# Optimization experiments

Measured on AMD Instinct MI355X. Metric: run time of the kernel, lower is better.

Reference implementation:

```python
import jax, jax.numpy as jnp
import numpy as np

# Module / shape constants (match init_kwargs and forward-path constants)
H = 8          # heads
DH = 80        # dim_head
QDIM = 640     # query_dim == inner_dim (context = x, self-attention content branch)
B = 1
NQ = 2048      # query tokens
NS = 2048      # injected style tokens
T = 1.2        # injection_config['T']  (attn_matrix_scale)
GAMMA = 0.3    # injection_config['gamma'] (q_mix)
LAMBDA_MAX = 2.5
TOPK = 128     # style_topk
STYLE_SCALE = 1.0
SCALE = DH ** -0.5


def _split_heads(t, h):
    # 'b n (h d) -> (b h) n d'
    b, n, hd = t.shape
    return t.reshape(b, n, h, hd // h).transpose(0, 2, 1, 3).reshape(b * h, n, hd // h)


def setup_inputs() -> dict:
    key = jax.random.key(0)
    ks = jax.random.split(key, 9)
    x = jax.random.normal(ks[0], (B, NQ, QDIM), jnp.float32)
    Q_c_injected = jax.random.normal(ks[1], (H, NQ, DH), jnp.float32) * 0.5
    K_s_injected = jax.random.normal(ks[2], (H, NS, DH), jnp.float32) * 0.5
    V_s_injected = jax.random.normal(ks[3], (H, NS, DH), jnp.float32) * 0.5
    # Learned params (nn.Linear weights are [out, in]; no bias on q/k/v)
    Wq = jax.random.normal(ks[4], (H * DH, QDIM), jnp.float32) * 0.02
    Wk = jax.random.normal(ks[5], (H * DH, QDIM), jnp.float32) * 0.02
    Wv = jax.random.normal(ks[6], (H * DH, QDIM), jnp.float32) * 0.02
    Wo = jax.random.normal(ks[7], (QDIM, H * DH), jnp.float32) * 0.02
    bo = jnp.zeros((QDIM,), jnp.float32)
    ada_gate = jnp.array([0.2], jnp.float32)
    return {"x": x, "Q_c_injected": Q_c_injected, "K_s_injected": K_s_injected,
            "V_s_injected": V_s_injected, "Wq": Wq, "Wk": Wk, "Wv": Wv,
            "Wo": Wo, "bo": bo, "ada_gate": ada_gate}


def reference(x, Q_c_injected, K_s_injected, V_s_injected, Wq, Wk, Wv, Wo, bo, ada_gate):
    b, n, _ = x.shape
    # Projections, context = x
    q_cs = _split_heads(x @ Wq.T, H)                    # (b h) n d
    k_cs = _split_heads(x @ Wk.T, H)                    # (b h) m d
    v_cs = _split_heads(x @ Wv.T, H)
    Q_c = jnp.tile(Q_c_injected, (b, 1, 1))             # torch.cat([Q_c]*b)
    q = Q_c * GAMMA + q_cs * (1.0 - GAMMA)              # Q_hat_cs
    K_s = jnp.tile(K_s_injected, (b, 1, 1))
    V_s = jnp.tile(V_s_injected, (b, 1, 1))

    style = jnp.einsum('bid,bjd->bij', q, K_s) * (T * SCALE)   # (bh) nq ns
    content = jnp.einsum('bid,bjd->bij', q, k_cs) * SCALE       # (bh) nq nc
    ns = style.shape[-1]
    s4 = style.reshape(b, H, n, ns)
    c4 = content.reshape(b, H, n, -1)

    # Per-head logsumexp gating between style and content branches
    r = jax.scipy.special.logsumexp(s4, axis=-1) - jax.scipy.special.logsumexp(c4, axis=-1)
    r = jnp.clip(r, -20.0, 20.0).mean(axis=1)           # (b, nq)
    lam = 1.0 + (LAMBDA_MAX - 1.0) * jax.nn.sigmoid(r)  # lambda_map
    style = (s4 * lam[:, None, :, None]).reshape(b * H, n, ns)

    # Top-k sparsification of style logits (scatter top-k values onto -inf canvas)
    vals, idx = jax.lax.top_k(style, TOPK)
    neg = jnp.finfo(style.dtype).min
    bi = jnp.arange(b * H)[:, None, None]
    ni = jnp.arange(n)[None, :, None]
    style = jnp.full_like(style, neg).at[bi, ni, idx].set(vals)

    logits = jnp.concatenate([style, content], axis=-1)
    attn = jax.nn.softmax(logits, axis=-1)
    v = jnp.concatenate([V_s * STYLE_SCALE, v_cs], axis=1)      # (bh) (ns+nc) d
    out = jnp.einsum('bij,bjd->bid', attn, v)

    # AdaIN-style modulation
    A = attn.reshape(b, H, n, -1)
    Vh = v.reshape(b, H, -1, DH)
    Qh = q.reshape(b, H, n, DH)
    Vmean = jnp.einsum('bhnm,bhmd->bhnd', A, Vh)
    mu = Qh.mean(axis=2, keepdims=True)
    var = Qh.var(axis=2, keepdims=True)                 # unbiased=False
    Qn = (Qh - mu) / jnp.sqrt(var + 1e-5)
    Vsq = jnp.einsum('bhnm,bhmd->bhnd', A, Vh * Vh)
    Vstd = jnp.sqrt(jnp.clip(Vsq - Vmean ** 2, 1e-5))
    out_mod = (Vstd * Qn + Vmean).reshape(b * H, n, DH)  # use_std_scale path

    g = jnp.tanh(ada_gate[0])                            # use_residual_gate
    out = out + g * (out_mod - out)
    out = out.reshape(b, H, n, DH).transpose(0, 2, 1, 3).reshape(b, n, H * DH)
    return out @ Wo.T + bo                               # to_out (dropout=0)
```

## Files before the change

### kernel.cpp

```cpp
#include <hip/hip_runtime.h>
#include <hip/hip_fp16.h>
#include <math.h>

#define NH 8
#define DH 80
#define NTOK 2048
#define QD 640
#define SCALE_F 0.11180339887498949f
#define TSCALE_F (1.2f * SCALE_F)
#define GAMMA_F 0.3f
#define LMAX_F 2.5f
#define TOPKN 128

typedef __attribute__((ext_vector_type(8))) short bf16x8;
typedef __attribute__((ext_vector_type(4))) float f32x4;
typedef __attribute__((ext_vector_type(4))) unsigned short u16x4;

#define OFF_QB   0u
#define OFF_OB   1310720u
#define OFF_QH   2621440u
#define OFF_QL   3407872u
#define OFF_KCH  4194304u
#define OFF_KSH  4980736u
#define OFF_KSL  5767168u
#define OFF_VCT  6553600u
#define OFF_VCQT 7208960u
#define OFF_VST  7864320u
#define OFF_VSQT 8519680u
#define OFF_OP   9175040u
#define OFF_SP   14417920u
#define OFF_DEN  19660800u
#define OFF_MSZ  19726336u
#define OFF_LSZ  19791872u
#define OFF_MCZ  19857408u
#define OFF_LCZ  19922944u
#define OFF_M    19988480u
#define OFF_LAM  20004864u
#define OFF_THR  20006912u
#define OFF_MU   20023296u
#define OFF_RSTD 20023936u
#define OFF_S16  20024576u
#define OFF_SC16 36801792u

static __device__ __forceinline__ unsigned short f2bf(float f) {
  unsigned u = __float_as_uint(f);
  return (unsigned short)((u + 0x7FFFu + ((u >> 16) & 1u)) >> 16);
}
static __device__ __forceinline__ float bf2f(unsigned short s) {
  return __uint_as_float(((unsigned)s) << 16);
}
static __device__ __forceinline__ unsigned sk16(unsigned u) {
  return (u & 0x8000u) ? (~u & 0xFFFFu) : (u | 0x8000u);
}

__global__ __launch_bounds__(256) void k_projmm(
    const float* __restrict__ x, const float* __restrict__ Wq,
    const float* __restrict__ Wk, const float* __restrict__ Wv,
    const float* __restrict__ Qc, float* __restrict__ qb,
    unsigned short* __restrict__ qh_, unsigned short* __restrict__ ql_,
    unsigned short* __restrict__ kch_,
    unsigned short* __restrict__ vct_, unsigned short* __restrict__ vcqt_)
{
  const float* W = (blockIdx.z == 0) ? Wq : ((blockIdx.z == 1) ? Wk : Wv);
  const int n0 = blockIdx.y * 64, c0 = blockIdx.x * 64;
  const int tid = threadIdx.x;
  const int w = tid >> 6, l = tid & 63;
  const int cc = l & 15, g = l >> 4;
  const bool full3 = (blockIdx.z == 0);

  __shared__ unsigned short sXh[64 * 72];
  __shared__ unsigned short sXl[64 * 72];
  __shared__ unsigned short sWh[64 * 72];
  __shared__ unsigned short sWl[64 * 72];

  f32x4 D[4];
#pragma unroll
  for (int ct = 0; ct < 4; ++ct) D[ct] = (f32x4){0.f, 0.f, 0.f, 0.f};

  for (int k0 = 0; k0 < QD; k0 += 64) {
    __syncthreads();
#pragma unroll
    for (int it = 0; it < 4; ++it) {
      int f = tid + it * 256;
      int row = f >> 4, col4 = f & 15;
      float4 xa = *(const float4*)(x + (size_t)(n0 + row) * QD + k0 + col4 * 4);
      float4 wa = *(const float4*)(W + (size_t)(c0 + row) * QD + k0 + col4 * 4);
      u16x4 xh, xl, wh, wl;
      float xv[4] = {xa.x, xa.y, xa.z, xa.w};
      float wv[4] = {wa.x, wa.y, wa.z, wa.w};
#pragma unroll
      for (int j = 0; j < 4; ++j) {
        unsigned short h1 = f2bf(xv[j]);
        xh[j] = h1; xl[j] = f2bf(xv[j] - bf2f(h1));
        unsigned short h2 = f2bf(wv[j]);
        wh[j] = h2; wl[j] = f2bf(wv[j] - bf2f(h2));
      }
      *(u16x4*)&sXh[row * 72 + col4 * 4] = xh;
      *(u16x4*)&sXl[row * 72 + col4 * 4] = xl;
      *(u16x4*)&sWh[row * 72 + col4 * 4] = wh;
      *(u16x4*)&sWl[row * 72 + col4 * 4] = wl;
    }
    __syncthreads();
    bf16x8 ah[2], al[2];
#pragma unroll
    for (int kc = 0; kc < 2; ++kc) {
      ah[kc] = *(const bf16x8*)&sXh[(w * 16 + cc) * 72 + kc * 32 + g * 8];
      al[kc] = *(const bf16x8*)&sXl[(w * 16 + cc) * 72 + kc * 32 + g * 8];
    }
#pragma unroll
    for (int ct = 0; ct < 4; ++ct) {
#pragma unroll
      for (int kc = 0; kc < 2; ++kc) {
        bf16x8 bh = *(const bf16x8*)&sWh[(ct * 16 + cc) * 72 + kc * 32 + g * 8];
        bf16x8 bl = *(const bf16x8*)&sWl[(ct * 16 + cc) * 72 + kc * 32 + g * 8];
        D[ct] = __builtin_amdgcn_mfma_f32_16x16x32_bf16(ah[kc], bh, D[ct], 0, 0, 0);
        D[ct] = __builtin_amdgcn_mfma_f32_16x16x32_bf16(ah[kc], bl, D[ct], 0, 0, 0);
        if (full3)
          D[ct] = __builtin_amdgcn_mfma_f32_16x16x32_bf16(al[kc], bh, D[ct], 0, 0, 0);
      }
    }
  }
#pragma unroll
  for (int ct = 0; ct < 4; ++ct) {
#pragma unroll
    for (int r = 0; r < 4; ++r) {
      int n = n0 + w * 16 + g * 4 + r;
      int ccol = c0 + ct * 16 + cc;
      int h = ccol / DH, d = ccol - h * DH;
      size_t i80 = ((size_t)h * NTOK + n) * 80 + d;
      size_t i96 = ((size_t)h * NTOK + n) * 96 + d;
      float val = D[ct][r];
      if (blockIdx.z == 0) {
        val = GAMMA_F * Qc[i80] + (1.f - GAMMA_F) * val;
        qb[i80] = val;
        unsigned short hs = f2bf(val);
        qh_[i96] = hs;
        ql_[i96] = f2bf(val - bf2f(hs));
      } else if (blockIdx.z == 1) {
        kch_[i96] = f2bf(val);
      } else {
        size_t iT = (((size_t)h * 80 + d) << 11) + n;
        vct_[iT]  = f2bf(val);
        vcqt_[iT] = f2bf(val * val);
      }
    }
  }
}

__global__ __launch_bounds__(256) void k_cvt(
    const float* __restrict__ Ks, const float* __restrict__ Vs,
    unsigned short* __restrict__ Ksh, unsigned short* __restrict__ Ksl,
    unsigned short* __restrict__ VTs, unsigned short* __restrict__ VTqs,
    unsigned short* __restrict__ qh_, unsigned short* __restrict__ ql_,
    unsigned short* __restrict__ kch_)
{
  const int h = blockIdx.y;
  const int n0 = blockIdx.x * 64;
  const int tid = threadIdx.x;
  __shared__ unsigned short sVT[80 * 68];
  __shared__ unsigned short sVQ[80 * 68];

  for (int f = tid; f < 1280; f += 256) {
    int rr = f / 20, dc = f % 20;
    size_t i80 = ((size_t)h * NTOK + n0 + rr) * 80 + dc * 4;
    size_t i96 = ((size_t)h * NTOK + n0 + rr) * 96 + dc * 4;
    float4 kv = *(const float4*)(Ks + i80);
    float kvv[4] = {kv.x, kv.y, kv.z, kv.w};
    u16x4 kh, kl;
#pragma unroll
    for (int j = 0; j < 4; ++j) {
      unsigned short hs = f2bf(kvv[j]);
      kh[j] = hs; kl[j] = f2bf(kvv[j] - bf2f(hs));
    }
    *(u16x4*)(Ksh + i96) = kh;
    *(u16x4*)(Ksl + i96) = kl;
    float4 vv = *(const float4*)(Vs + i80);
    float vvv[4] = {vv.x, vv.y, vv.z, vv.w};
#pragma unroll
    for (int j = 0; j < 4; ++j) {
      int d = dc * 4 + j;
      sVT[d * 68 + rr] = f2bf(vvv[j]);
      sVQ[d * 68 + rr] = f2bf(vvv[j] * vvv[j]);
    }
  }
  for (int f = tid; f < 1024; f += 256) {
    int rr = f >> 4, dcol = 80 + (f & 15);
    size_t i96 = ((size_t)h * NTOK + n0 + rr) * 96 + dcol;
    Ksh[i96] = 0; Ksl[i96] = 0; qh_[i96] = 0; ql_[i96] = 0; kch_[i96] = 0;
  }
  __syncthreads();
  for (int f = tid; f < 640; f += 256) {
    int d = f >> 3, kp8 = f & 7;
    size_t iT = (((size_t)h * 80 + d) << 11) + n0 + kp8 * 8;
    *(bf16x8*)(VTs + iT)  = *(const bf16x8*)&sVT[d * 68 + kp8 * 8];
    *(bf16x8*)(VTqs + iT) = *(const bf16x8*)&sVQ[d * 68 + kp8 * 8];
  }
}

__global__ __launch_bounds__(128) void k_qstats(
    const float* __restrict__ qb, float* __restrict__ mu, float* __restrict__ rstd)
{
  const int h = blockIdx.x / DH, d = blockIdx.x % DH;
  const int tid = threadIdx.x;
  float s = 0.f, s2 = 0.f;
  for (int n = tid; n < NTOK; n += 128) {
    float v = qb[((size_t)h * NTOK + n) * 80 + d];
    s += v; s2 = fmaf(v, v, s2);
  }
#pragma unroll
  for (int off = 32; off; off >>= 1) { s += __shfl_xor(s, off, 64); s2 += __shfl_xor(s2, off, 64); }
  __shared__ float sh[4];
  if ((tid & 63) == 0) { sh[(tid >> 6) * 2] = s; sh[(tid >> 6) * 2 + 1] = s2; }
  __syncthreads();
  if (tid == 0) {
    float S = sh[0] + sh[2], S2 = sh[1] + sh[3];
    float mval = S * (1.f / NTOK);
    float var = S2 * (1.f / NTOK) - mval * mval;
    mu[h * DH + d] = mval;
    rstd[h * DH + d] = rsqrtf(var + 1e-5f);
  }
}

__global__ __launch_bounds__(256) void k_passA(
    const unsigned short* __restrict__ qh_, const unsigned short* __restrict__ ql_,
    const unsigned short* __restrict__ Ksh, const unsigned short* __restrict__ Ksl,
    const unsigned short* __restrict__ kch_,
    unsigned short* __restrict__ S16, unsigned short* __restrict__ Sc16,
    float* __restrict__ mSz, float* __restrict__ lSz,
    float* __restrict__ mCz, float* __restrict__ lCz)
{
  const int bid = blockIdx.x;
  const int swz = (bid & 7) * 128 + (bid >> 3);
  const int q0 = (swz & 31) * 64;
  const int h  = (swz >> 5) & 7;
  const int z  = swz >> 8;
  const int tid = threadIdx.x;
  const int w = tid >> 6, l = tid & 63;
  const int c = l & 15, g = l >> 4;

  __shared__ unsigned short sKh[64 * 104];
  __shared__ unsigned short sKl[64 * 104];
  __shared__ unsigned short sS[4 * 16 * 68];
  unsigned short* sSw = sS + w * 16 * 68;
  const int orow = l >> 2, oq = l & 3;

  bf16x8 qhf[3], qlf[3];
  {
    const size_t qrow = ((size_t)h * NTOK + q0 + w * 16 + c) * 96;
#pragma unroll
    for (int kc = 0; kc < 3; ++kc) {
      qhf[kc] = *(const bf16x8*)(qh_ + qrow + kc * 32 + g * 8);
      qlf[kc] = *(const bf16x8*)(ql_ + qrow + kc * 32 + g * 8);
    }
  }
  float m[4], lse[4], mc[4], lc[4];
#pragma unroll
  for (int r = 0; r < 4; ++r) { m[r] = -INFINITY; lse[r] = 0.f; mc[r] = -INFINITY; lc[r] = 0.f; }

  for (int t = 0; t < 8; ++t) {
    const size_t kbase = ((size_t)h * NTOK + z * 512 + t * 64) * 96;
    __syncthreads();
    for (int f = tid; f < 768; f += 256) {
      int row = f / 12, ch = f % 12;
      *(bf16x8*)(sKh + row * 104 + ch * 8) = *(const bf16x8*)(Ksh + kbase + row * 96 + ch * 8);
      *(bf16x8*)(sKl + row * 104 + ch * 8) = *(const bf16x8*)(Ksl + kbase + row * 96 + ch * 8);
    }
    __syncthreads();
#pragma unroll
    for (int ct = 0; ct < 4; ++ct) {
      f32x4 D = {0.f, 0.f, 0.f, 0.f};
      const int krow = (ct * 16 + c) * 104 + g * 8;
#pragma unroll
      for (int kc = 0; kc < 3; ++kc) {
        bf16x8 bh = *(const bf16x8*)(sKh + krow + kc * 32);
        D = __builtin_amdgcn_mfma_f32_16x16x32_bf16(qhf[kc], bh, D, 0, 0, 0);
      }
#pragma unroll
      for (int kc = 0; kc < 3; ++kc) {
        bf16x8 bl = *(const bf16x8*)(sKl + krow + kc * 32);
        D = __builtin_amdgcn_mfma_f32_16x16x32_bf16(qhf[kc], bl, D, 0, 0, 0);
      }
#pragma unroll
      for (int kc = 0; kc < 3; ++kc) {
        bf16x8 bh = *(const bf16x8*)(sKh + krow + kc * 32);
        D = __builtin_amdgcn_mfma_f32_16x16x32_bf16(qlf[kc], bh, D, 0, 0, 0);
      }
#pragma unroll
      for (int r = 0; r < 4; ++r) {
        float s = D[r] * TSCALE_F;
        sSw[(g * 4 + r) * 68 + ct * 16 + c] = __half_as_ushort(__float2half(s));
        lse[r] += __expf(s);
        m[r] = fmaxf(m[r], s);
      }
    }
    {
      size_t gbase = ((size_t)h * NTOK + q0 + w * 16 + orow) * 2048 + z * 512 + t * 64 + oq * 16;
      *(uint4*)(S16 + gbase)     = *(const uint4*)&sSw[orow * 68 + oq * 16];
      *(uint4*)(S16 + gbase + 8) = *(const uint4*)&sSw[orow * 68 + oq * 16 + 8];
    }
  }
  for (int t = 0; t < 8; ++t) {
    const size_t kbase = ((size_t)h * NTOK + z * 512 + t * 64) * 96;
    __syncthreads();
    for (int f = tid; f < 768; f += 256) {
      int row = f / 12, ch = f % 12;
      *(bf16x8*)(sKh + row * 104 + ch * 8) = *(const bf16x8*)(kch_ + kbase + row * 96 + ch * 8);
    }
    __syncthreads();
#pragma unroll
    for (int ct = 0; ct < 4; ++ct) {
      f32x4 D = {0.f, 0.f, 0.f, 0.f};
      const int krow = (ct * 16 + c) * 104 + g * 8;
#pragma unroll
      for (int kc = 0; kc < 3; ++kc) {
        bf16x8 bh = *(const bf16x8*)(sKh + krow + kc * 32);
        D = __builtin_amdgcn_mfma_f32_16x16x32_bf16(qhf[kc], bh, D, 0, 0, 0);
      }
#pragma unroll
      for (int r = 0; r < 4; ++r) {
        float s = D[r] * SCALE_F;
        sSw[(g * 4 + r) * 68 + ct * 16 + c] = __half_as_ushort(__float2half(s));
        lc[r] += __expf(s);
        mc[r] = fmaxf(mc[r], s);
      }
    }
    {
      size_t gbase = ((size_t)h * NTOK + q0 + w * 16 + orow) * 2048 + z * 512 + t * 64 + oq * 16;
      *(uint4*)(Sc16 + gbase)     = *(const uint4*)&sSw[orow * 68 + oq * 16];
      *(uint4*)(Sc16 + gbase + 8) = *(const uint4*)&sSw[orow * 68 + oq * 16 + 8];
    }
  }
#pragma unroll
  for (int off = 1; off < 16; off <<= 1) {
#pragma unroll
    for (int r = 0; r < 4; ++r) {
      lse[r] += __shfl_xor(lse[r], off, 64);
      m[r] = fmaxf(m[r], __shfl_xor(m[r], off, 64));
      lc[r] += __shfl_xor(lc[r], off, 64);
      mc[r] = fmaxf(mc[r], __shfl_xor(mc[r], off, 64));
    }
  }
  if (c == 0) {
    size_t base = (size_t)(z * 8 + h) * NTOK + q0 + w * 16 + g * 4;
#pragma unroll
    for (int r = 0; r < 4; ++r) {
      mSz[base + r] = m[r]; lSz[base + r] = lse[r];
      mCz[base + r] = mc[r]; lCz[base + r] = lc[r];
    }
  }
}

__global__ __launch_bounds__(256) void k_gate(
    const float* __restrict__ mSz, const float* __restrict__ lSz,
    const float* __restrict__ mCz, const float* __restrict__ lCz,
    float* __restrict__ M_, float* __restrict__ lam_)
{
  int n = blockIdx.x * 256 + threadIdx.x;
  if (n >= NTOK) return;
  float msf[NH], mcf[NH], sum = 0.f;
#pragma unroll
  for (int h = 0; h < NH; ++h) {
    float mm = -INFINITY, cm = -INFINITY, ls = 0.f, lcs = 0.f;
#pragma unroll
    for (int zz = 0; zz < 4; ++zz) {
      mm = fmaxf(mm, mSz[(size_t)(zz * 8 + h) * NTOK + n]);
      cm = fmaxf(cm, mCz[(size_t)(zz * 8 + h) * NTOK + n]);
      ls  += lSz[(size_t)(zz * 8 + h) * NTOK + n];
      lcs += lCz[(size_t)(zz * 8 + h) * NTOK + n];
    }
    float lse_s = __logf(ls);
    float lse_c = __logf(lcs);
    msf[h] = mm; mcf[h] = cm;
    sum += fminf(fmaxf(lse_s - lse_c, -20.f), 20.f);
  }
  float lam = 1.f + (LMAX_F - 1.f) * (1.f / (1.f + __expf(-sum * (1.f / NH))));
  lam_[n] = lam;
#pragma unroll
  for (int h = 0; h < NH; ++h)
    M_[h * NTOK + n] = fmaxf(lam * msf[h], mcf[h]);
}

__global__ __launch_bounds__(512) void k_topk(const unsigned short* __restrict__ S16,
                                              unsigned* __restrict__ thr_)
{
  const int h = blockIdx.y;
  const int n = blockIdx.x * 8 + (threadIdx.x >> 6);
  const int l = threadIdx.x & 63;
  const unsigned short* Srow = S16 + ((size_t)h * NTOK + n) * 2048;
  unsigned kv[32];
#pragma unroll
  for (int t = 0; t < 4; ++t) {
    uint4 v = ((const uint4*)Srow)[t * 64 + l];
    unsigned dw[4] = {v.x, v.y, v.z, v.w};
#pragma unroll
    for (int i = 0; i < 8; ++i) {
      unsigned u = (dw[i >> 1] >> ((i & 1) * 16)) & 0xFFFFu;
      kv[t * 8 + i] = sk16(u);
    }
  }
  unsigned klo = 0u, khi = 65536u;
  for (int it = 0; it < 16; ++it) {
    unsigned mid = (klo + khi) >> 1;
    int cnt = 0;
#pragma unroll
    for (int t = 0; t < 32; ++t)
      cnt += __popcll(__ballot(kv[t] >= mid));
    if (cnt == TOPKN) { klo = mid; break; }
    if (cnt > TOPKN) klo = mid; else khi = mid;
    if (khi - klo <= 1u) break;
  }
  if (l == 0) thr_[h * NTOK + n] = klo;
}

__global__ __launch_bounds__(256) void k_passB(
    const unsigned short* __restrict__ VTs, const unsigned short* __restrict__ VTqs,
    const unsigned short* __restrict__ VTc, const unsigned short* __restrict__ VTqc,
    const unsigned short* __restrict__ S16, const unsigned short* __restrict__ Sc16,
    const float* __restrict__ M_, const float* __restrict__ lam_,
    const unsigned* __restrict__ thr_,
    float* __restrict__ oP, float* __restrict__ sP, float* __restrict__ denP)
{
  const int bid = blockIdx.x;
  const int swz = (bid & 7) * 128 + (bid >> 3);
  const int q0 = (swz & 31) * 64;
  const int h  = (swz >> 5) & 7;
  const int z  = swz >> 8;
  const int tid = threadIdx.x;
  const int w = tid >> 6, l = tid & 63;
  const int c = l & 15, g = l >> 4;

  __shared__ unsigned short vT[80 * 72];
  __shared__ unsigned short vqT[80 * 72];

  const int myrow = w * 16 + c;
  const float myM = M_[h * NTOK + q0 + myrow];
  const float myLam = lam_[q0 + myrow];
  const unsigned myThr = thr_[h * NTOK + q0 + myrow];

  const size_t srow = ((size_t)h * NTOK + q0 + myrow) * 2048 + g * 8;
  const int d0 = tid >> 3, kp8 = tid & 7;
  const size_t vr0 = (((size_t)h * 80 + d0) << 11) + kp8 * 8;
  const size_t vr1 = (((size_t)h * 80 + d0 + 32) << 11) + kp8 * 8;
  const size_t vr2 = (((size_t)h * 80 + d0 + 64) << 11) + kp8 * 8;
  const bool third = (tid < 128);

  f32x4 oacc[5], sacc[5];
#pragma unroll
  for (int dt = 0; dt < 5; ++dt) { oacc[dt] = (f32x4){0.f,0.f,0.f,0.f}; sacc[dt] = (f32x4){0.f,0.f,0.f,0.f}; }
  float den = 0.f;

  for (int t = 0; t < 16; ++t) {
    const bool style = (t < 8);
    const int k0 = z * 512 + (t & 7) * 64;
    const unsigned short* Sp = style ? S16 : Sc16;
    const unsigned short* Vp = style ? VTs : VTc;
    const unsigned short* Vq = style ? VTqs : VTqc;
    uint4 s0 = *(const uint4*)(Sp + srow + k0);
    uint4 s1 = *(const uint4*)(Sp + srow + k0 + 32);
    bf16x8 v0 = *(const bf16x8*)(Vp + vr0 + k0);
    bf16x8 v1 = *(const bf16x8*)(Vp + vr1 + k0);
    bf16x8 u0 = *(const bf16x8*)(Vq + vr0 + k0);
    bf16x8 u1 = *(const bf16x8*)(Vq + vr1 + k0);
    bf16x8 v2, u2;
    if (third) {
      v2 = *(const bf16x8*)(Vp + vr2 + k0);
      u2 = *(const bf16x8*)(Vq + vr2 + k0);
    }
    __syncthreads();
    *(bf16x8*)&vT[d0 * 72 + kp8 * 8] = v0;
    *(bf16x8*)&vqT[d0 * 72 + kp8 * 8] = u0;
    *(bf16x8*)&vT[(d0 + 32) * 72 + kp8 * 8] = v1;
    *(bf16x8*)&vqT[(d0 + 32) * 72 + kp8 * 8] = u1;
    if (third) {
      *(bf16x8*)&vT[(d0 + 64) * 72 + kp8 * 8] = v2;
      *(bf16x8*)&vqT[(d0 + 64) * 72 + kp8 * 8] = u2;
    }
    __syncthreads();
    bf16x8 pa0, pa1;
    {
      unsigned dw0[4] = {s0.x, s0.y, s0.z, s0.w};
      unsigned dw1[4] = {s1.x, s1.y, s1.z, s1.w};
#pragma unroll
      for (int i = 0; i < 8; ++i) {
        unsigned ua = (dw0[i >> 1] >> ((i & 1) * 16)) & 0xFFFFu;
        float sa = __half2float(__ushort_as_half((unsigned short)ua));
        float wa = style ? ((sk16(ua) >= myThr) ? __expf(myLam * sa - myM) : 0.f)
                         : __expf(sa - myM);
        den += wa;
        pa0[i] = (short)f2bf(wa);
        unsigned ub = (dw1[i >> 1] >> ((i & 1) * 16)) & 0xFFFFu;
        float sb = __half2float(__ushort_as_half((unsigned short)ub));
        float wb = style ? ((sk16(ub) >= myThr) ? __expf(myLam * sb - myM) : 0.f)
                         : __expf(sb - myM);
        den += wb;
        pa1[i] = (short)f2bf(wb);
      }
    }
#pragma unroll
    for (int dt = 0; dt < 5; ++dt) {
      bf16x8 bv0  = *(const bf16x8*)&vT[(dt * 16 + c) * 72 + g * 8];
      bf16x8 bvq0 = *(const bf16x8*)&vqT[(dt * 16 + c) * 72 + g * 8];
      bf16x8 bv1  = *(const bf16x8*)&vT[(dt * 16 + c) * 72 + 32 + g * 8];
      bf16x8 bvq1 = *(const bf16x8*)&vqT[(dt * 16 + c) * 72 + 32 + g * 8];
      oacc[dt] = __builtin_amdgcn_mfma_f32_16x16x32_bf16(pa0, bv0, oacc[dt], 0, 0, 0);
      sacc[dt] = __builtin_amdgcn_mfma_f32_16x16x32_bf16(pa0, bvq0, sacc[dt], 0, 0, 0);
      oacc[dt] = __builtin_amdgcn_mfma_f32_16x16x32_bf16(pa1, bv1, oacc[dt], 0, 0, 0);
      sacc[dt] = __builtin_amdgcn_mfma_f32_16x16x32_bf16(pa1, bvq1, sacc[dt], 0, 0, 0);
    }
  }
  den += __shfl_xor(den, 16, 64);
  den += __shfl_xor(den, 32, 64);
  if (g == 0) denP[(size_t)(z * 8 + h) * NTOK + q0 + myrow] = den;
  const size_t base = (size_t)(z * 8 + h) * NTOK + q0 + w * 16;
#pragma unroll
  for (int dt = 0; dt < 5; ++dt)
#pragma unroll
    for (int r = 0; r < 4; ++r) {
      size_t o = (base + g * 4 + r) * 80 + dt * 16 + c;
      oP[o] = oacc[dt][r];
      sP[o] = sacc[dt][r];
    }
}

__global__ __launch_bounds__(256) void k_fin(
    const float* __restrict__ oP, const float* __restrict__ sP,
    const float* __restrict__ denP, const float* __restrict__ qb,
    const float* __restrict__ mu, const float* __restrict__ rstd,
    const float* __restrict__ gate, float* __restrict__ Ob)
{
  int idx = blockIdx.x * 256 + threadIdx.x;
  int h = idx / (NTOK * 80);
  int rem = idx - h * (NTOK * 80);
  int n = rem / 80, d = rem - n * 80;
  float den = 0.f, o = 0.f, sq = 0.f;
#pragma unroll
  for (int zz = 0; zz < 4; ++zz) {
    den += denP[(size_t)(zz * 8 + h) * NTOK + n];
    size_t p = ((size_t)(zz * 8 + h) * NTOK + n) * 80 + d;
    o += oP[p];
    sq += sP[p];
  }
  o /= den;
  sq /= den;
  float vstd = sqrtf(fmaxf(sq - o * o, 1e-5f));
  float g = tanhf(gate[0]);
  float qn = (qb[((size_t)h * NTOK + n) * 80 + d] - mu[h * DH + d]) * rstd[h * DH + d];
  Ob[(size_t)n * QD + h * DH + d] = fmaf(g * vstd, qn, o);
}

__global__ __launch_bounds__(256) void k_finalmm(
    const float* __restrict__ A, const float* __restrict__ W,
    const float* __restrict__ bias, float* __restrict__ out)
{
  const int n0 = blockIdx.y * 64, c0 = blockIdx.x * 64;
  const int tid = threadIdx.x;
  const int w = tid >> 6, l = tid & 63;
  const int cc = l & 15, g = l >> 4;

  __shared__ unsigned short sXh[64 * 72];
  __shared__ unsigned short sXl[64 * 72];
  __shared__ unsigned short sWh[64 * 72];
  __shared__ unsigned short sWl[64 * 72];

  f32x4 D[4];
#pragma unroll
  for (int ct = 0; ct < 4; ++ct) D[ct] = (f32x4){0.f, 0.f, 0.f, 0.f};

  for (int k0 = 0; k0 < QD; k0 += 64) {
    __syncthreads();
#pragma unroll
    for (int it = 0; it < 4; ++it) {
      int f = tid + it * 256;
      int row = f >> 4, col4 = f & 15;
      float4 xa = *(const float4*)(A + (size_t)(n0 + row) * QD + k0 + col4 * 4);
      float4 wa = *(const float4*)(W + (size_t)(c0 + row) * QD + k0 + col4 * 4);
      u16x4 xh, xl, wh, wl;
      float xv[4] = {xa.x, xa.y, xa.z, xa.w};
      float wv[4] = {wa.x, wa.y, wa.z, wa.w};
#pragma unroll
      for (int j = 0; j < 4; ++j) {
        unsigned short h1 = f2bf(xv[j]);
        xh[j] = h1; xl[j] = f2bf(xv[j] - bf2f(h1));
        unsigned short h2 = f2bf(wv[j]);
        wh[j] = h2; wl[j] = f2bf(wv[j] - bf2f(h2));
      }
      *(u16x4*)&sXh[row * 72 + col4 * 4] = xh;
      *(u16x4*)&sXl[row * 72 + col4 * 4] = xl;
      *(u16x4*)&sWh[row * 72 + col4 * 4] = wh;
      *(u16x4*)&sWl[row * 72 + col4 * 4] = wl;
    }
    __syncthreads();
    bf16x8 ah[2], al[2];
#pragma unroll
    for (int kc = 0; kc < 2; ++kc) {
      ah[kc] = *(const bf16x8*)&sXh[(w * 16 + cc) * 72 + kc * 32 + g * 8];
      al[kc] = *(const bf16x8*)&sXl[(w * 16 + cc) * 72 + kc * 32 + g * 8];
    }
#pragma unroll
    for (int ct = 0; ct < 4; ++ct) {
#pragma unroll
      for (int kc = 0; kc < 2; ++kc) {
        bf16x8 bh = *(const bf16x8*)&sWh[(ct * 16 + cc) * 72 + kc * 32 + g * 8];
        bf16x8 bl = *(const bf16x8*)&sWl[(ct * 16 + cc) * 72 + kc * 32 + g * 8];
        D[ct] = __builtin_amdgcn_mfma_f32_16x16x32_bf16(ah[kc], bh, D[ct], 0, 0, 0);
        D[ct] = __builtin_amdgcn_mfma_f32_16x16x32_bf16(ah[kc], bl, D[ct], 0, 0, 0);
        D[ct] = __builtin_amdgcn_mfma_f32_16x16x32_bf16(al[kc], bh, D[ct], 0, 0, 0);
      }
    }
  }
#pragma unroll
  for (int ct = 0; ct < 4; ++ct) {
#pragma unroll
    for (int r = 0; r < 4; ++r) {
      int n = n0 + w * 16 + g * 4 + r;
      int ccol = c0 + ct * 16 + cc;
      out[(size_t)n * QD + ccol] = D[ct][r] + bias[ccol];
    }
  }
}

extern "C" void kernel_launch(void* const* d_in, const int* in_sizes, int n_in,
                              void* d_out, int out_size, void* d_ws, size_t ws_size,
                              hipStream_t stream) {
  const float* x    = (const float*)d_in[0];
  const float* Qc   = (const float*)d_in[1];
  const float* Ks   = (const float*)d_in[2];
  const float* Vs   = (const float*)d_in[3];
  const float* Wq   = (const float*)d_in[4];
  const float* Wk   = (const float*)d_in[5];
  const float* Wv   = (const float*)d_in[6];
  const float* Wo   = (const float*)d_in[7];
  const float* bo   = (const float*)d_in[8];
  const float* gate = (const float*)d_in[9];
  float* out = (float*)d_out;
  float* w = (float*)d_ws;

  float* qb   = w + OFF_QB;
  float* Ob   = w + OFF_OB;
  unsigned short* qh_  = (unsigned short*)(w + OFF_QH);
  unsigned short* ql_  = (unsigned short*)(w + OFF_QL);
  unsigned short* kch_ = (unsigned short*)(w + OFF_KCH);
  unsigned short* Ksh  = (unsigned short*)(w + OFF_KSH);
  unsigned short* Ksl  = (unsigned short*)(w + OFF_KSL);
  unsigned short* VTc  = (unsigned short*)(w + OFF_VCT);
  unsigned short* VTqc = (unsigned short*)(w + OFF_VCQT);
  unsigned short* VTs  = (unsigned short*)(w + OFF_VST);
  unsigned short* VTqs = (unsigned short*)(w + OFF_VSQT);
  float* oP   = w + OFF_OP;
  float* sP   = w + OFF_SP;
  float* denP = w + OFF_DEN;
  float* mSz  = w + OFF_MSZ;
  float* lSz  = w + OFF_LSZ;
  float* mCz  = w + OFF_MCZ;
  float* lCz  = w + OFF_LCZ;
  float* M_   = w + OFF_M;
  float* lam_ = w + OFF_LAM;
  unsigned* thr_ = (unsigned*)(w + OFF_THR);
  float* mu   = w + OFF_MU;
  float* rstd = w + OFF_RSTD;
  unsigned short* S16  = (unsigned short*)(w + OFF_S16);
  unsigned short* Sc16 = (unsigned short*)(w + OFF_SC16);

  k_projmm<<<dim3(10, 32, 3), 256, 0, stream>>>(x, Wq, Wk, Wv, Qc, qb, qh_, ql_, kch_, VTc, VTqc);
  k_cvt<<<dim3(32, 8), 256, 0, stream>>>(Ks, Vs, Ksh, Ksl, VTs, VTqs, qh_, ql_, kch_);
  k_qstats<<<dim3(640), 128, 0, stream>>>(qb, mu, rstd);
  k_passA<<<dim3(1024), 256, 0, stream>>>(qh_, ql_, Ksh, Ksl, kch_, S16, Sc16, mSz, lSz, mCz, lCz);
  k_gate<<<dim3(8), 256, 0, stream>>>(mSz, lSz, mCz, lCz, M_, lam_);
  k_topk<<<dim3(256, 8), 512, 0, stream>>>(S16, thr_);
  k_passB<<<dim3(1024), 256, 0, stream>>>(VTs, VTqs, VTc, VTqc, S16, Sc16, M_, lam_, thr_, oP, sP, denP);
  k_fin<<<dim3(5120), 256, 0, stream>>>(oP, sP, denP, qb, mu, rstd, gate, Ob);
  k_finalmm<<<dim3(10, 32), 256, 0, stream>>>(Ob, Wo, bo, out);
}
```

Baseline: 253.4 us.

## Double key-split count, store fp16 partials, write score tiles directly

Splits the key dimension into eight chunks instead of four, doubling the number of blocks in both attention passes to raise parallelism. Partial output and squared-value accumulators are stored as fp16 to halve their traffic, and passA writes scores straight to global memory instead of staging through shared memory. Risks include uncoalesced 2-byte stores, more partial reduction work in the finish kernel, and fp16 range or precision loss on unnormalized accumulators.

```diff
diff --git a/kernel.cpp b/kernel.cpp
--- a/kernel.cpp
+++ b/kernel.cpp
@@ -11,6 +11,7 @@
 #define GAMMA_F 0.3f
 #define LMAX_F 2.5f
 #define TOPKN 128
+#define NZ 8
 
 typedef __attribute__((ext_vector_type(8))) short bf16x8;
 typedef __attribute__((ext_vector_type(4))) float f32x4;
@@ -30,17 +31,17 @@
 #define OFF_OP   9175040u
 #define OFF_SP   14417920u
 #define OFF_DEN  19660800u
-#define OFF_MSZ  19726336u
-#define OFF_LSZ  19791872u
-#define OFF_MCZ  19857408u
-#define OFF_LCZ  19922944u
-#define OFF_M    19988480u
-#define OFF_LAM  20004864u
-#define OFF_THR  20006912u
-#define OFF_MU   20023296u
-#define OFF_RSTD 20023936u
-#define OFF_S16  20024576u
-#define OFF_SC16 36801792u
+#define OFF_MSZ  19791872u
+#define OFF_LSZ  19922944u
+#define OFF_MCZ  20054016u
+#define OFF_LCZ  20185088u
+#define OFF_M    20316160u
+#define OFF_LAM  20332544u
+#define OFF_THR  20334592u
+#define OFF_MU   20350976u
+#define OFF_RSTD 20351616u
+#define OFF_S16  20352256u
+#define OFF_SC16 37129472u
 
 static __device__ __forceinline__ unsigned short f2bf(float f) {
   unsigned u = __float_as_uint(f);
@@ -230,7 +231,7 @@
     float* __restrict__ mCz, float* __restrict__ lCz)
 {
   const int bid = blockIdx.x;
-  const int swz = (bid & 7) * 128 + (bid >> 3);
+  const int swz = (bid & 7) * 256 + (bid >> 3);
   const int q0 = (swz & 31) * 64;
   const int h  = (swz >> 5) & 7;
   const int z  = swz >> 8;
@@ -240,9 +241,6 @@
 
   __shared__ unsigned short sKh[64 * 104];
   __shared__ unsigned short sKl[64 * 104];
-  __shared__ unsigned short sS[4 * 16 * 68];
-  unsigned short* sSw = sS + w * 16 * 68;
-  const int orow = l >> 2, oq = l & 3;
 
   bf16x8 qhf[3], qlf[3];
   {
@@ -257,8 +255,8 @@
 #pragma unroll
   for (int r = 0; r < 4; ++r) { m[r] = -INFINITY; lse[r] = 0.f; mc[r] = -INFINITY; lc[r] = 0.f; }
 
-  for (int t = 0; t < 8; ++t) {
-    const size_t kbase = ((size_t)h * NTOK + z * 512 + t * 64) * 96;
+  for (int t = 0; t < 4; ++t) {
+    const size_t kbase = ((size_t)h * NTOK + z * 256 + t * 64) * 96;
     __syncthreads();
     for (int f = tid; f < 768; f += 256) {
       int row = f / 12, ch = f % 12;
@@ -288,19 +286,15 @@
 #pragma unroll
       for (int r = 0; r < 4; ++r) {
         float s = D[r] * TSCALE_F;
-        sSw[(g * 4 + r) * 68 + ct * 16 + c] = __half_as_ushort(__float2half(s));
+        S16[((size_t)h * NTOK + q0 + w * 16 + g * 4 + r) * 2048 + z * 256 + t * 64 + ct * 16 + c] =
+            __half_as_ushort(__float2half(s));
         lse[r] += __expf(s);
         m[r] = fmaxf(m[r], s);
       }
     }
-    {
-      size_t gbase = ((size_t)h * NTOK + q0 + w * 16 + orow) * 2048 + z * 512 + t * 64 + oq * 16;
-      *(uint4*)(S16 + gbase)     = *(const uint4*)&sSw[orow * 68 + oq * 16];
-      *(uint4*)(S16 + gbase + 8) = *(const uint4*)&sSw[orow * 68 + oq * 16 + 8];
-    }
-  }
-  for (int t = 0; t < 8; ++t) {
-    const size_t kbase = ((size_t)h * NTOK + z * 512 + t * 64) * 96;
+  }
+  for (int t = 0; t < 4; ++t) {
+    const size_t kbase = ((size_t)h * NTOK + z * 256 + t * 64) * 96;
     __syncthreads();
     for (int f = tid; f < 768; f += 256) {
       int row = f / 12, ch = f % 12;
@@ -319,15 +313,11 @@
 #pragma unroll
       for (int r = 0; r < 4; ++r) {
         float s = D[r] * SCALE_F;
-        sSw[(g * 4 + r) * 68 + ct * 16 + c] = __half_as_ushort(__float2half(s));
+        Sc16[((size_t)h * NTOK + q0 + w * 16 + g * 4 + r) * 2048 + z * 256 + t * 64 + ct * 16 + c] =
+            __half_as_ushort(__float2half(s));
         lc[r] += __expf(s);
         mc[r] = fmaxf(mc[r], s);
       }
-    }
-    {
-      size_t gbase = ((size_t)h * NTOK + q0 + w * 16 + orow) * 2048 + z * 512 + t * 64 + oq * 16;
-      *(uint4*)(Sc16 + gbase)     = *(const uint4*)&sSw[orow * 68 + oq * 16];
-      *(uint4*)(Sc16 + gbase + 8) = *(const uint4*)&sSw[orow * 68 + oq * 16 + 8];
     }
   }
 #pragma unroll
@@ -362,7 +352,7 @@
   for (int h = 0; h < NH; ++h) {
     float mm = -INFINITY, cm = -INFINITY, ls = 0.f, lcs = 0.f;
 #pragma unroll
-    for (int zz = 0; zz < 4; ++zz) {
+    for (int zz = 0; zz < NZ; ++zz) {
       mm = fmaxf(mm, mSz[(size_t)(zz * 8 + h) * NTOK + n]);
       cm = fmaxf(cm, mCz[(size_t)(zz * 8 + h) * NTOK + n]);
       ls  += lSz[(size_t)(zz * 8 + h) * NTOK + n];
@@ -418,10 +408,11 @@
     const unsigned short* __restrict__ S16, const unsigned short* __restrict__ Sc16,
     const float* __restrict__ M_, const float* __restrict__ lam_,
     const unsigned* __restrict__ thr_,
-    float* __restrict__ oP, float* __restrict__ sP, float* __restrict__ denP)
+    unsigned short* __restrict__ oP, unsigned short* __restrict__ sP,
+    float* __restrict__ denP)
 {
   const int bid = blockIdx.x;
-  const int swz = (bid & 7) * 128 + (bid >> 3);
+  const int swz = (bid & 7) * 256 + (bid >> 3);
   const int q0 = (swz & 31) * 64;
   const int h  = (swz >> 5) & 7;
   const int z  = swz >> 8;
@@ -449,9 +440,9 @@
   for (int dt = 0; dt < 5; ++dt) { oacc[dt] = (f32x4){0.f,0.f,0.f,0.f}; sacc[dt] = (f32x4){0.f,0.f,0.f,0.f}; }
   float den = 0.f;
 
-  for (int t = 0; t < 16; ++t) {
-    const bool style = (t < 8);
-    const int k0 = z * 512 + (t & 7) * 64;
+  for (int t = 0; t < 8; ++t) {
+    const bool style = (t < 4);
+    const int k0 = z * 256 + (t & 3) * 64;
     const unsigned short* Sp = style ? S16 : Sc16;
     const unsigned short* Vp = style ? VTs : VTc;
     const unsigned short* Vq = style ? VTqs : VTqc;
@@ -517,13 +508,13 @@
 #pragma unroll
     for (int r = 0; r < 4; ++r) {
       size_t o = (base + g * 4 + r) * 80 + dt * 16 + c;
-      oP[o] = oacc[dt][r];
-      sP[o] = sacc[dt][r];
+      oP[o] = __half_as_ushort(__float2half(oacc[dt][r]));
+      sP[o] = __half_as_ushort(__float2half(sacc[dt][r]));
     }
 }
 
 __global__ __launch_bounds__(256) void k_fin(
-    const float* __restrict__ oP, const float* __restrict__ sP,
+    const unsigned short* __restrict__ oP, const unsigned short* __restrict__ sP,
     const float* __restrict__ denP, const float* __restrict__ qb,
     const float* __restrict__ mu, const float* __restrict__ rstd,
     const float* __restrict__ gate, float* __restrict__ Ob)
@@ -534,11 +525,11 @@
   int n = rem / 80, d = rem - n * 80;
   float den = 0.f, o = 0.f, sq = 0.f;
 #pragma unroll
-  for (int zz = 0; zz < 4; ++zz) {
+  for (int zz = 0; zz < NZ; ++zz) {
     den += denP[(size_t)(zz * 8 + h) * NTOK + n];
     size_t p = ((size_t)(zz * 8 + h) * NTOK + n) * 80 + d;
-    o += oP[p];
-    sq += sP[p];
+    o += __half2float(__ushort_as_half(oP[p]));
+    sq += __half2float(__ushort_as_half(sP[p]));
   }
   o /= den;
   sq /= den;
@@ -646,8 +637,8 @@
   unsigned short* VTqc = (unsigned short*)(w + OFF_VCQT);
   unsigned short* VTs  = (unsigned short*)(w + OFF_VST);
   unsigned short* VTqs = (unsigned short*)(w + OFF_VSQT);
-  float* oP   = w + OFF_OP;
-  float* sP   = w + OFF_SP;
+  unsigned short* oP   = (unsigned short*)(w + OFF_OP);
+  unsigned short* sP   = (unsigned short*)(w + OFF_SP);
   float* denP = w + OFF_DEN;
   float* mSz  = w + OFF_MSZ;
   float* lSz  = w + OFF_LSZ;
@@ -664,10 +655,10 @@
   k_projmm<<<dim3(10, 32, 3), 256, 0, stream>>>(x, Wq, Wk, Wv, Qc, qb, qh_, ql_, kch_, VTc, VTqc);
   k_cvt<<<dim3(32, 8), 256, 0, stream>>>(Ks, Vs, Ksh, Ksl, VTs, VTqs, qh_, ql_, kch_);
   k_qstats<<<dim3(640), 128, 0, stream>>>(qb, mu, rstd);
-  k_passA<<<dim3(1024), 256, 0, stream>>>(qh_, ql_, Ksh, Ksl, kch_, S16, Sc16, mSz, lSz, mCz, lCz);
+  k_passA<<<dim3(2048), 256, 0, stream>>>(qh_, ql_, Ksh, Ksl, kch_, S16, Sc16, mSz, lSz, mCz, lCz);
   k_gate<<<dim3(8), 256, 0, stream>>>(mSz, lSz, mCz, lCz, M_, lam_);
   k_topk<<<dim3(256, 8), 512, 0, stream>>>(S16, thr_);
-  k_passB<<<dim3(1024), 256, 0, stream>>>(VTs, VTqs, VTc, VTqc, S16, Sc16, M_, lam_, thr_, oP, sP, denP);
+  k_passB<<<dim3(2048), 256, 0, stream>>>(VTs, VTqs, VTc, VTqc, S16, Sc16, M_, lam_, thr_, oP, sP, denP);
   k_fin<<<dim3(5120), 256, 0, stream>>>(oP, sP, denP, qb, mu, rstd, gate, Ob);
   k_finalmm<<<dim3(10, 32), 256, 0, stream>>>(Ob, Wo, bo, out);
 }
```

New measurement: 297.9 us. +17.6%, slower.

## Recompute content logits in passB instead of storing fp16 content scores

Applied to the files above, without the earlier changes.

Pass A stops writing the fp16 content score matrix (H x 2048 x 2048) to global memory and keeps only its max and sum statistics. Pass B now splits its loop into a style phase and a content phase. The content phase reloads the q and K_c tiles, recomputes the scores with MFMA, exponentiates them and routes them through LDS into the PV MFMA layout. This removes a large global write plus read in exchange for duplicated QK^T compute, more LDS traffic and extra syncs in pass B.

```diff
diff --git a/kernel.cpp b/kernel.cpp
--- a/kernel.cpp
+++ b/kernel.cpp
@@ -40,7 +40,6 @@
 #define OFF_MU   20023296u
 #define OFF_RSTD 20023936u
 #define OFF_S16  20024576u
-#define OFF_SC16 36801792u
 
 static __device__ __forceinline__ unsigned short f2bf(float f) {
   unsigned u = __float_as_uint(f);
@@ -225,7 +224,7 @@
     const unsigned short* __restrict__ qh_, const unsigned short* __restrict__ ql_,
     const unsigned short* __restrict__ Ksh, const unsigned short* __restrict__ Ksl,
     const unsigned short* __restrict__ kch_,
-    unsigned short* __restrict__ S16, unsigned short* __restrict__ Sc16,
+    unsigned short* __restrict__ S16,
     float* __restrict__ mSz, float* __restrict__ lSz,
     float* __restrict__ mCz, float* __restrict__ lCz)
 {
@@ -319,15 +318,9 @@
 #pragma unroll
       for (int r = 0; r < 4; ++r) {
         float s = D[r] * SCALE_F;
-        sSw[(g * 4 + r) * 68 + ct * 16 + c] = __half_as_ushort(__float2half(s));
         lc[r] += __expf(s);
         mc[r] = fmaxf(mc[r], s);
       }
-    }
-    {
-      size_t gbase = ((size_t)h * NTOK + q0 + w * 16 + orow) * 2048 + z * 512 + t * 64 + oq * 16;
-      *(uint4*)(Sc16 + gbase)     = *(const uint4*)&sSw[orow * 68 + oq * 16];
-      *(uint4*)(Sc16 + gbase + 8) = *(const uint4*)&sSw[orow * 68 + oq * 16 + 8];
     }
   }
 #pragma unroll
@@ -413,9 +406,10 @@
 }
 
 __global__ __launch_bounds__(256) void k_passB(
+    const unsigned short* __restrict__ qh_, const unsigned short* __restrict__ kch_,
     const unsigned short* __restrict__ VTs, const unsigned short* __restrict__ VTqs,
     const unsigned short* __restrict__ VTc, const unsigned short* __restrict__ VTqc,
-    const unsigned short* __restrict__ S16, const unsigned short* __restrict__ Sc16,
+    const unsigned short* __restrict__ S16,
     const float* __restrict__ M_, const float* __restrict__ lam_,
     const unsigned* __restrict__ thr_,
     float* __restrict__ oP, float* __restrict__ sP, float* __restrict__ denP)
@@ -429,13 +423,29 @@
   const int w = tid >> 6, l = tid & 63;
   const int c = l & 15, g = l >> 4;
 
-  __shared__ unsigned short vT[80 * 72];
-  __shared__ unsigned short vqT[80 * 72];
+  __shared__ char arena[36352];
+  unsigned short* kch_lds = (unsigned short*)arena;
+  unsigned short* P_lds   = (unsigned short*)arena;
+  unsigned short* vT      = (unsigned short*)(arena + 13312);
+  unsigned short* vqT     = (unsigned short*)(arena + 24832);
+  __shared__ float den_l[64];
 
   const int myrow = w * 16 + c;
   const float myM = M_[h * NTOK + q0 + myrow];
   const float myLam = lam_[q0 + myrow];
   const unsigned myThr = thr_[h * NTOK + q0 + myrow];
+  float myM4[4];
+#pragma unroll
+  for (int r = 0; r < 4; ++r) myM4[r] = M_[h * NTOK + q0 + w * 16 + g * 4 + r];
+
+  bf16x8 qhf[3];
+  {
+    const size_t qrow = ((size_t)h * NTOK + q0 + w * 16 + c) * 96;
+#pragma unroll
+    for (int kc = 0; kc < 3; ++kc)
+      qhf[kc] = *(const bf16x8*)(qh_ + qrow + kc * 32 + g * 8);
+  }
+  if (tid < 64) den_l[tid] = 0.f;
 
   const size_t srow = ((size_t)h * NTOK + q0 + myrow) * 2048 + g * 8;
   const int d0 = tid >> 3, kp8 = tid & 7;
@@ -447,24 +457,20 @@
   f32x4 oacc[5], sacc[5];
 #pragma unroll
   for (int dt = 0; dt < 5; ++dt) { oacc[dt] = (f32x4){0.f,0.f,0.f,0.f}; sacc[dt] = (f32x4){0.f,0.f,0.f,0.f}; }
-  float den = 0.f;
-
-  for (int t = 0; t < 16; ++t) {
-    const bool style = (t < 8);
-    const int k0 = z * 512 + (t & 7) * 64;
-    const unsigned short* Sp = style ? S16 : Sc16;
-    const unsigned short* Vp = style ? VTs : VTc;
-    const unsigned short* Vq = style ? VTqs : VTqc;
-    uint4 s0 = *(const uint4*)(Sp + srow + k0);
-    uint4 s1 = *(const uint4*)(Sp + srow + k0 + 32);
-    bf16x8 v0 = *(const bf16x8*)(Vp + vr0 + k0);
-    bf16x8 v1 = *(const bf16x8*)(Vp + vr1 + k0);
-    bf16x8 u0 = *(const bf16x8*)(Vq + vr0 + k0);
-    bf16x8 u1 = *(const bf16x8*)(Vq + vr1 + k0);
+  float denS = 0.f, denC[4] = {0.f, 0.f, 0.f, 0.f};
+
+  for (int t = 0; t < 8; ++t) {
+    const int k0 = z * 512 + t * 64;
+    uint4 s0 = *(const uint4*)(S16 + srow + k0);
+    uint4 s1 = *(const uint4*)(S16 + srow + k0 + 32);
+    bf16x8 v0 = *(const bf16x8*)(VTs + vr0 + k0);
+    bf16x8 v1 = *(const bf16x8*)(VTs + vr1 + k0);
+    bf16x8 u0 = *(const bf16x8*)(VTqs + vr0 + k0);
+    bf16x8 u1 = *(const bf16x8*)(VTqs + vr1 + k0);
     bf16x8 v2, u2;
     if (third) {
-      v2 = *(const bf16x8*)(Vp + vr2 + k0);
-      u2 = *(const bf16x8*)(Vq + vr2 + k0);
+      v2 = *(const bf16x8*)(VTs + vr2 + k0);
+      u2 = *(const bf16x8*)(VTqs + vr2 + k0);
     }
     __syncthreads();
     *(bf16x8*)&vT[d0 * 72 + kp8 * 8] = v0;
@@ -484,15 +490,13 @@
       for (int i = 0; i < 8; ++i) {
         unsigned ua = (dw0[i >> 1] >> ((i & 1) * 16)) & 0xFFFFu;
         float sa = __half2float(__ushort_as_half((unsigned short)ua));
-        float wa = style ? ((sk16(ua) >= myThr) ? __expf(myLam * sa - myM) : 0.f)
-                         : __expf(sa - myM);
-        den += wa;
+        float wa = (sk16(ua) >= myThr) ? __expf(myLam * sa - myM) : 0.f;
+        denS += wa;
         pa0[i] = (short)f2bf(wa);
         unsigned ub = (dw1[i >> 1] >> ((i & 1) * 16)) & 0xFFFFu;
         float sb = __half2float(__ushort_as_half((unsigned short)ub));
-        float wb = style ? ((sk16(ub) >= myThr) ? __expf(myLam * sb - myM) : 0.f)
-                         : __expf(sb - myM);
-        den += wb;
+        float wb = (sk16(ub) >= myThr) ? __expf(myLam * sb - myM) : 0.f;
+        denS += wb;
         pa1[i] = (short)f2bf(wb);
       }
     }
@@ -508,9 +512,86 @@
       sacc[dt] = __builtin_amdgcn_mfma_f32_16x16x32_bf16(pa1, bvq1, sacc[dt], 0, 0, 0);
     }
   }
-  den += __shfl_xor(den, 16, 64);
-  den += __shfl_xor(den, 32, 64);
-  if (g == 0) denP[(size_t)(z * 8 + h) * NTOK + q0 + myrow] = den;
+  denS += __shfl_xor(denS, 16, 64);
+  denS += __shfl_xor(denS, 32, 64);
+  if (g == 0) den_l[myrow] = denS;
+
+  for (int t = 0; t < 8; ++t) {
+    const int k0 = z * 512 + t * 64;
+    const size_t kbase = ((size_t)h * NTOK + k0) * 96;
+    bf16x8 v0 = *(const bf16x8*)(VTc + vr0 + k0);
+    bf16x8 v1 = *(const bf16x8*)(VTc + vr1 + k0);
+    bf16x8 u0 = *(const bf16x8*)(VTqc + vr0 + k0);
+    bf16x8 u1 = *(const bf16x8*)(VTqc + vr1 + k0);
+    bf16x8 v2, u2;
+    if (third) {
+      v2 = *(const bf16x8*)(VTc + vr2 + k0);
+      u2 = *(const bf16x8*)(VTqc + vr2 + k0);
+    }
+    __syncthreads();
+    for (int f = tid; f < 768; f += 256) {
+      int row = f / 12, ch = f % 12;
+      *(bf16x8*)(kch_lds + row * 104 + ch * 8) =
+          *(const bf16x8*)(kch_ + kbase + row * 96 + ch * 8);
+    }
+    *(bf16x8*)&vT[d0 * 72 + kp8 * 8] = v0;
+    *(bf16x8*)&vqT[d0 * 72 + kp8 * 8] = u0;
+    *(bf16x8*)&vT[(d0 + 32) * 72 + kp8 * 8] = v1;
+    *(bf16x8*)&vqT[(d0 + 32) * 72 + kp8 * 8] = u1;
+    if (third) {
+      *(bf16x8*)&vT[(d0 + 64) * 72 + kp8 * 8] = v2;
+      *(bf16x8*)&vqT[(d0 + 64) * 72 + kp8 * 8] = u2;
+    }
+    __syncthreads();
+    unsigned short pv[4][4];
+#pragma unroll
+    for (int ct = 0; ct < 4; ++ct) {
+      f32x4 D = {0.f, 0.f, 0.f, 0.f};
+      const int krow = (ct * 16 + c) * 104 + g * 8;
+#pragma unroll
+      for (int kc = 0; kc < 3; ++kc) {
+        bf16x8 bh = *(const bf16x8*)(kch_lds + krow + kc * 32);
+        D = __builtin_amdgcn_mfma_f32_16x16x32_bf16(qhf[kc], bh, D, 0, 0, 0);
+      }
+#pragma unroll
+      for (int r = 0; r < 4; ++r) {
+        float s = D[r] * SCALE_F;
+        float wv = __expf(s - myM4[r]);
+        denC[r] += wv;
+        pv[ct][r] = f2bf(wv);
+      }
+    }
+    __syncthreads();
+#pragma unroll
+    for (int ct = 0; ct < 4; ++ct)
+#pragma unroll
+      for (int r = 0; r < 4; ++r)
+        P_lds[w * 1152 + (g * 4 + r) * 72 + ct * 16 + c] = pv[ct][r];
+    bf16x8 pa0 = *(const bf16x8*)(P_lds + w * 1152 + c * 72 + g * 8);
+    bf16x8 pa1 = *(const bf16x8*)(P_lds + w * 1152 + c * 72 + 32 + g * 8);
+#pragma unroll
+    for (int dt = 0; dt < 5; ++dt) {
+      bf16x8 bv0  = *(const bf16x8*)&vT[(dt * 16 + c) * 72 + g * 8];
+      bf16x8 bvq0 = *(const bf16x8*)&vqT[(dt * 16 + c) * 72 + g * 8];
+      bf16x8 bv1  = *(const bf16x8*)&vT[(dt * 16 + c) * 72 + 32 + g * 8];
+      bf16x8 bvq1 = *(const bf16x8*)&vqT[(dt * 16 + c) * 72 + 32 + g * 8];
+      oacc[dt] = __builtin_amdgcn_mfma_f32_16x16x32_bf16(pa0, bv0, oacc[dt], 0, 0, 0);
+      sacc[dt] = __builtin_amdgcn_mfma_f32_16x16x32_bf16(pa0, bvq0, sacc[dt], 0, 0, 0);
+      oacc[dt] = __builtin_amdgcn_mfma_f32_16x16x32_bf16(pa1, bv1, oacc[dt], 0, 0, 0);
+      sacc[dt] = __builtin_amdgcn_mfma_f32_16x16x32_bf16(pa1, bvq1, sacc[dt], 0, 0, 0);
+    }
+  }
+#pragma unroll
+  for (int off = 1; off < 16; off <<= 1)
+#pragma unroll
+    for (int r = 0; r < 4; ++r) denC[r] += __shfl_xor(denC[r], off, 64);
+  __syncthreads();
+  if (c == 0) {
+#pragma unroll
+    for (int r = 0; r < 4; ++r) den_l[w * 16 + g * 4 + r] += denC[r];
+  }
+  __syncthreads();
+  if (tid < 64) denP[(size_t)(z * 8 + h) * NTOK + q0 + tid] = den_l[tid];
   const size_t base = (size_t)(z * 8 + h) * NTOK + q0 + w * 16;
 #pragma unroll
   for (int dt = 0; dt < 5; ++dt)
@@ -659,15 +740,14 @@
   float* mu   = w + OFF_MU;
   float* rstd = w + OFF_RSTD;
   unsigned short* S16  = (unsigned short*)(w + OFF_S16);
-  unsigned short* Sc16 = (unsigned short*)(w + OFF_SC16);
 
   k_projmm<<<dim3(10, 32, 3), 256, 0, stream>>>(x, Wq, Wk, Wv, Qc, qb, qh_, ql_, kch_, VTc, VTqc);
   k_cvt<<<dim3(32, 8), 256, 0, stream>>>(Ks, Vs, Ksh, Ksl, VTs, VTqs, qh_, ql_, kch_);
   k_qstats<<<dim3(640), 128, 0, stream>>>(qb, mu, rstd);
-  k_passA<<<dim3(1024), 256, 0, stream>>>(qh_, ql_, Ksh, Ksl, kch_, S16, Sc16, mSz, lSz, mCz, lCz);
+  k_passA<<<dim3(1024), 256, 0, stream>>>(qh_, ql_, Ksh, Ksl, kch_, S16, mSz, lSz, mCz, lCz);
   k_gate<<<dim3(8), 256, 0, stream>>>(mSz, lSz, mCz, lCz, M_, lam_);
   k_topk<<<dim3(256, 8), 512, 0, stream>>>(S16, thr_);
-  k_passB<<<dim3(1024), 256, 0, stream>>>(VTs, VTqs, VTc, VTqc, S16, Sc16, M_, lam_, thr_, oP, sP, denP);
+  k_passB<<<dim3(1024), 256, 0, stream>>>(qh_, kch_, VTs, VTqs, VTc, VTqc, S16, M_, lam_, thr_, oP, sP, denP);
   k_fin<<<dim3(5120), 256, 0, stream>>>(oP, sP, denP, qb, mu, rstd, gate, Ob);
   k_finalmm<<<dim3(10, 32), 256, 0, stream>>>(Ob, Wo, bo, out);
 }
```

After: 264.9 us. +4.5%, slower.
